# Optimization experiments

Measured on AMD Instinct MI355X. Metric: run time of the kernel, lower is better.

Reference implementation:

```python
import jax, jax.numpy as jnp
import numpy as np
import math

NUM_POSE_FEAT = 64  # -> pos emb dim 128
N_NBR = 16
TEMP = 10000.0


def pos2posemb2d(pos, num_pos_feats=NUM_POSE_FEAT):
    # PETR-style 2D sine embedding; pos: (..., 2) in [0,1)
    scale = 2.0 * math.pi
    pos = pos * scale
    dim_t = jnp.arange(num_pos_feats, dtype=pos.dtype)
    dim_t = TEMP ** (2.0 * jnp.floor(dim_t / 2.0) / num_pos_feats)
    pos_x = pos[..., 0:1] / dim_t  # (..., P)
    pos_y = pos[..., 1:2] / dim_t

    def interleave(p):
        return jnp.stack([jnp.sin(p[..., 0::2]), jnp.cos(p[..., 1::2])], axis=-1).reshape(p.shape[:-1] + (-1,))

    return jnp.concatenate([interleave(pos_y), interleave(pos_x)], axis=-1)  # (..., 2P)


def mlp(x, W1, b1, W2, b2):
    return jax.nn.relu(x @ W1 + b1) @ W2 + b2


def setup_inputs() -> dict:
    key = jax.random.key(0)
    ks = jax.random.split(key, 12)
    B, S, L, D, P2 = 4, 4096, 8192, 256, 2 * NUM_POSE_FEAT
    s1 = 1.0 / np.sqrt(P2)
    s2 = 1.0 / np.sqrt(D)
    return {
        "memory": jax.random.normal(ks[0], (B, L, D), jnp.float32),
        "mem_coor": jax.random.uniform(ks[1], (B, L, 2), dtype=jnp.float32),
        "q_coor": jax.random.uniform(ks[2], (B, S, 2), dtype=jnp.float32),
        "Wq1": jax.random.normal(ks[3], (P2, D), jnp.float32) * s1,
        "bq1": jnp.zeros((D,), jnp.float32),
        "Wq2": jax.random.normal(ks[4], (D, D), jnp.float32) * s2,
        "bq2": jnp.zeros((D,), jnp.float32),
        "Wk1": jax.random.normal(ks[5], (P2, D), jnp.float32) * s1,
        "bk1": jnp.zeros((D,), jnp.float32),
        "Wk2": jax.random.normal(ks[6], (D, D), jnp.float32) * s2,
        "bk2": jnp.zeros((D,), jnp.float32),
        "B": 4,
    }


def reference(memory, mem_coor, q_coor, Wq1, bq1, Wq2, bq2, Wk1, bk1, Wk2, bk2, B):
    # memory: (B, L, D); mem_coor: (B, L, 2); q_coor: (B, S, 2)
    Bn, L, D = memory.shape
    query = mlp(pos2posemb2d(q_coor), Wq1, bq1, Wq2, bq2)      # (B, S, D) query = query_pos
    mem_pos = mlp(pos2posemb2d(mem_coor), Wk1, bk1, Wk2, bk2)  # (B, L, D)
    kv_pe = mem_pos + memory                                   # (B, L, D)

    # squared pairwise distances via matmul expansion (monotonic in true distance,
    # only the top-k ORDER is consumed downstream)
    q2 = jnp.sum(q_coor * q_coor, axis=-1)                     # (B, S)
    m2 = jnp.sum(mem_coor * mem_coor, axis=-1)                 # (B, L)
    d2 = q2[:, :, None] + m2[:, None, :] - 2.0 * jnp.einsum("bsc,blc->bsl", q_coor, mem_coor)
    _, idx = jax.lax.top_k(-d2, N_NBR)                         # (B, S, k) nearest-neighbor indices

    bidx = jnp.arange(Bn)[:, None, None]
    kv_m = kv_pe[bidx, idx]                                    # (B, S, k, D) gathered pos-embedded memory
    prod = query[:, :, None, :] * kv_m / jnp.sqrt(jnp.asarray(D, query.dtype))
    attn = jax.nn.softmax(prod, axis=-1)                       # softmax over feature dim D
    out = attn * memory[bidx, idx]                             # (B, S, k, D)
    return out
```

## Files before the change

kernel.cpp:

```cpp
#include <hip/hip_runtime.h>
#include <math.h>

#define NB 4
#define NS 4096
#define NL 8192
#define ND 256
#define NP2 128
#define NK 16

#define GCELLS 32
#define GH 0.03125f
#define CAP 256
#define EPSM 2e-5f

__device__ __forceinline__ float sum_sq_np(float x, float y) {
#pragma clang fp contract(off)
  return x * x + y * y;
}

__device__ __forceinline__ float dist2_fast(float q2, float m2, float qx, float qy,
                                            float mx, float my) {
#pragma clang fp contract(off)
  float dot = __builtin_fmaf(qy, my, qx * mx);
  float s = q2 + m2;
  return __builtin_fmaf(-2.0f, dot, s);
}

__device__ __forceinline__ unsigned f32ord(float f) {
  unsigned u = __float_as_uint(f);
  return u ^ ((unsigned)((int)u >> 31) | 0x80000000u);
}

template <int NR>
__device__ __forceinline__ unsigned extract16(const unsigned long long* candrow,
                                              int cnt, int lane,
                                              int* __restrict__ outp) {
  unsigned long long myc[NR];
#pragma unroll
  for (int j = 0; j < NR; ++j) {
    int p = lane + j * 64;
    myc[j] = (p < cnt) ? candrow[p] : ~0ull;
  }
  unsigned tau_ord = 0xffffffffu;
#pragma unroll 1
  for (int r = 0; r < NK; ++r) {
    unsigned long long m = myc[0];
#pragma unroll
    for (int j = 1; j < NR; ++j) m = myc[j] < m ? myc[j] : m;
#pragma unroll
    for (int o = 1; o < 64; o <<= 1) {
      unsigned long long other = __shfl_xor(m, o, 64);
      if (other < m) m = other;
    }
    if (lane == 0) outp[r] = (int)(unsigned)(m & 0xffffffffull);
    if (r == NK - 1) tau_ord = (unsigned)(m >> 32);
#pragma unroll
    for (int j = 0; j < NR; ++j)
      if (myc[j] == m) myc[j] = ~0ull;
  }
  return tau_ord;
}

#define RPAD 20
#define NSBLK (NB * NS / 16)

struct __align__(16) MlpSmem {
  float pe[NP2][RPAD];
  float h[ND][RPAD];
};

__device__ __forceinline__ void fma16(float* acc, float wt, const float4& p0,
                                      const float4& p1, const float4& p2,
                                      const float4& p3) {
  acc[0] = fmaf(p0.x, wt, acc[0]);   acc[1] = fmaf(p0.y, wt, acc[1]);
  acc[2] = fmaf(p0.z, wt, acc[2]);   acc[3] = fmaf(p0.w, wt, acc[3]);
  acc[4] = fmaf(p1.x, wt, acc[4]);   acc[5] = fmaf(p1.y, wt, acc[5]);
  acc[6] = fmaf(p1.z, wt, acc[6]);   acc[7] = fmaf(p1.w, wt, acc[7]);
  acc[8] = fmaf(p2.x, wt, acc[8]);   acc[9] = fmaf(p2.y, wt, acc[9]);
  acc[10] = fmaf(p2.z, wt, acc[10]); acc[11] = fmaf(p2.w, wt, acc[11]);
  acc[12] = fmaf(p3.x, wt, acc[12]); acc[13] = fmaf(p3.y, wt, acc[13]);
  acc[14] = fmaf(p3.z, wt, acc[14]); acc[15] = fmaf(p3.w, wt, acc[15]);
}

__device__ __forceinline__ void loadW8(const float* __restrict__ W, int k0,
                                       int tid, float* w0, float* w1) {
#pragma unroll
  for (int u = 0; u < 8; ++u) {
    w0[u] = W[(size_t)(k0 + u) * ND + tid];
    w1[u] = W[(size_t)(k0 + u) * ND + 128 + tid];
  }
}

__device__ __forceinline__ void consume8(const float (*L)[RPAD], int k0,
                                         const float* w0, const float* w1,
                                         float* acc0, float* acc1) {
#pragma unroll
  for (int u = 0; u < 8; ++u) {
    int k = k0 + u;
    float4 p0 = *(const float4*)&L[k][0];
    float4 p1 = *(const float4*)&L[k][4];
    float4 p2 = *(const float4*)&L[k][8];
    float4 p3 = *(const float4*)&L[k][12];
    fma16(acc0, w0[u], p0, p1, p2, p3);
    fma16(acc1, w1[u], p0, p1, p2, p3);
  }
}

__global__ __launch_bounds__(128) void mlp_fused_kernel(
    const float* __restrict__ q_coor, const float* __restrict__ mem_coor,
    const float* __restrict__ memory,
    const float* __restrict__ Wq1, const float* __restrict__ bq1,
    const float* __restrict__ Wq2, const float* __restrict__ bq2,
    const float* __restrict__ Wk1, const float* __restrict__ bk1,
    const float* __restrict__ Wk2, const float* __restrict__ bk2,
    float* __restrict__ query, float* __restrict__ kv_pe) {
  __shared__ MlpSmem sm;
  const int tid = threadIdx.x;
  const int bid = blockIdx.x;
  const bool isS = bid < NSBLK;
  const float* coor = isS ? q_coor : mem_coor;
  const float* W1 = isS ? Wq1 : Wk1;
  const float* b1 = isS ? bq1 : bk1;
  const float* W2 = isS ? Wq2 : Wk2;
  const float* b2 = isS ? bq2 : bk2;
  const float* addmem = isS ? (const float*)nullptr : memory;
  float* out = isS ? query : kv_pe;
  const int row0 = (isS ? bid : bid - NSBLK) * 16;

#pragma unroll
  for (int it = 0; it < 8; ++it) {
    int e = tid + it * 128;
    int r = e >> 6;
    int rem = e & 63;
    int part = rem >> 5;
    int j = rem & 31;
    float c = coor[(size_t)(row0 + r) * 2 + (part ^ 1)];
    float inv_t = exp2f((float)j * -0.4152410118609718f);
    float arg = c * 6.2831853071795864f * inv_t;
    float sv, cv;
    sincosf(arg, &sv, &cv);
    int k0 = part * 64 + 2 * j;
    sm.pe[k0][r] = sv;
    sm.pe[k0 + 1][r] = cv;
  }
  __syncthreads();

  float acc0[16], acc1[16];
  float wA0[8], wA1[8], wB0[8], wB1[8];
  {
    float bb0 = b1[tid], bb1 = b1[tid + 128];
#pragma unroll
    for (int r = 0; r < 16; ++r) { acc0[r] = bb0; acc1[r] = bb1; }
  }
  loadW8(W1, 0, tid, wA0, wA1);
#pragma unroll 1
  for (int k0 = 0; k0 < NP2; k0 += 16) {
    loadW8(W1, k0 + 8, tid, wB0, wB1);
    consume8(sm.pe, k0, wA0, wA1, acc0, acc1);
    if (k0 + 16 < NP2) loadW8(W1, k0 + 16, tid, wA0, wA1);
    consume8(sm.pe, k0 + 8, wB0, wB1, acc0, acc1);
  }
#pragma unroll
  for (int r = 0; r < 16; ++r) {
    sm.h[tid][r] = fmaxf(acc0[r], 0.0f);
    sm.h[tid + 128][r] = fmaxf(acc1[r], 0.0f);
  }
  __syncthreads();

  {
    float bb0 = b2[tid], bb1 = b2[tid + 128];
#pragma unroll
    for (int r = 0; r < 16; ++r) { acc0[r] = bb0; acc1[r] = bb1; }
  }
  loadW8(W2, 0, tid, wA0, wA1);
#pragma unroll 1
  for (int k0 = 0; k0 < ND; k0 += 16) {
    loadW8(W2, k0 + 8, tid, wB0, wB1);
    consume8(sm.h, k0, wA0, wA1, acc0, acc1);
    if (k0 + 16 < ND) loadW8(W2, k0 + 16, tid, wA0, wA1);
    consume8(sm.h, k0 + 8, wB0, wB1, acc0, acc1);
  }
#pragma unroll
  for (int r = 0; r < 16; ++r) {
    size_t g = (size_t)(row0 + r);
    float v0 = acc0[r], v1 = acc1[r];
    if (addmem) {
      v0 += addmem[g * ND + tid];
      v1 += addmem[g * ND + 128 + tid];
    }
    out[g * ND + tid] = v0;
    out[g * ND + 128 + tid] = v1;
  }
}

__global__ __launch_bounds__(1024) void grid_build_kernel(
    const float* __restrict__ mem_coor, float4* __restrict__ sorted,
    int* __restrict__ starts) {
  __shared__ int hist[GCELLS * GCELLS];
  __shared__ int cur[GCELLS * GCELLS];
  const int b = blockIdx.x;
  const int tid = threadIdx.x;
  const float2* mc = (const float2*)mem_coor + (size_t)b * NL;

  hist[tid] = 0;
  __syncthreads();
#pragma unroll
  for (int it = 0; it < NL / 1024; ++it) {
    float2 c = mc[it * 1024 + tid];
    int cx = (int)(c.x * 32.0f); cx = cx > 31 ? 31 : cx;
    int cy = (int)(c.y * 32.0f); cy = cy > 31 ? 31 : cy;
    atomicAdd(&hist[cy * GCELLS + cx], 1);
  }
  __syncthreads();
  const int own = hist[tid];
  for (int o = 1; o < 1024; o <<= 1) {
    int v = (tid >= o) ? hist[tid - o] : 0;
    __syncthreads();
    hist[tid] += v;
    __syncthreads();
  }
  const int excl = hist[tid] - own;
  starts[b * (GCELLS * GCELLS + 1) + tid] = excl;
  if (tid == 0) starts[b * (GCELLS * GCELLS + 1) + GCELLS * GCELLS] = NL;
  cur[tid] = excl;
  __syncthreads();
#pragma unroll
  for (int it = 0; it < NL / 1024; ++it) {
    int i = it * 1024 + tid;
    float2 c = mc[i];
    int cx = (int)(c.x * 32.0f); cx = cx > 31 ? 31 : cx;
    int cy = (int)(c.y * 32.0f); cy = cy > 31 ? 31 : cy;
    int pos = atomicAdd(&cur[cy * GCELLS + cx], 1);
    sorted[(size_t)b * NL + pos] =
        make_float4(c.x, c.y, sum_sq_np(c.x, c.y), __int_as_float(i));
  }
}

__global__ __launch_bounds__(256) void topk_kernel(
    const float* __restrict__ q_coor, const float4* __restrict__ sorted,
    const int* __restrict__ starts, int* __restrict__ idx_out) {
  __shared__ unsigned long long cand[4][CAP];
  __shared__ int fcnt[4];

  const int tid = threadIdx.x;
  const int wv = tid >> 6;
  const int lane = tid & 63;
  const int qi = blockIdx.x * 4 + wv;
  const int b = qi >> 12;

  const float qx = q_coor[(size_t)qi * 2 + 0];
  const float qy = q_coor[(size_t)qi * 2 + 1];
  const float q2 = sum_sq_np(qx, qy);
  const float4* sp = sorted + (size_t)b * NL;
  const int* st = starts + b * (GCELLS * GCELLS + 1);
  int* outp = idx_out + (size_t)qi * NK;

  int ci = (int)(qx * 32.0f); ci = ci > 31 ? 31 : ci;
  int cj = (int)(qy * 32.0f); cj = cj > 31 ? 31 : cj;

  int x0 = ci - 1 < 0 ? 0 : ci - 1, x1 = ci + 1 > 31 ? 31 : ci + 1;
  int y0 = cj - 1 < 0 ? 0 : cj - 1, y1 = cj + 1 > 31 ? 31 : cj + 1;
  int cnt = 0;
  bool ovf = false;

  auto span = [&](int y, int xa, int xb) {
    int s0 = st[y * GCELLS + xa];
    int e0 = st[y * GCELLS + xb + 1];
    int len = e0 - s0;
    if (cnt + len > CAP) { ovf = true; return; }
    for (int i = lane; i < len; i += 64) {
      float4 rx = sp[s0 + i];
      float d2 = dist2_fast(q2, rx.z, qx, qy, rx.x, rx.y);
      cand[wv][cnt + i] = ((unsigned long long)f32ord(d2) << 32) |
                          (unsigned)__float_as_int(rx.w);
    }
    cnt += len;
  };

  for (int y = y0; y <= y1 && !ovf; ++y) span(y, x0, x1);

  int R = 1;
  while (!ovf) {
    unsigned tau_ord;
    if (cnt <= 128) tau_ord = extract16<2>(cand[wv], cnt, lane, outp);
    else            tau_ord = extract16<4>(cand[wv], cnt, lane, outp);
    float dxl = x0 > 0  ? qx - (float)x0 * GH        : 1e30f;
    float dxr = x1 < 31 ? (float)(x1 + 1) * GH - qx  : 1e30f;
    float dyl = y0 > 0  ? qy - (float)y0 * GH        : 1e30f;
    float dyr = y1 < 31 ? (float)(y1 + 1) * GH - qy  : 1e30f;
    float dmin = fminf(fminf(dxl, dxr), fminf(dyl, dyr));
    float bound = dmin * dmin - EPSM;
    if (cnt >= NK && tau_ord < f32ord(bound)) return;
    if (x0 == 0 && x1 == 31 && y0 == 0 && y1 == 31) return;
    ++R;
    int nx0 = ci - R < 0 ? 0 : ci - R, nx1 = ci + R > 31 ? 31 : ci + R;
    int ny0 = cj - R < 0 ? 0 : cj - R, ny1 = cj + R > 31 ? 31 : cj + R;
    if (ny0 < y0) span(ny0, nx0, nx1);
    if (ny1 > y1 && !ovf) span(ny1, nx0, nx1);
    for (int y = y0; y <= y1 && !ovf; ++y) {
      if (nx0 < x0) span(y, nx0, x0 - 1);
      if (nx1 > x1 && !ovf) span(y, x1 + 1, nx1);
    }
    x0 = nx0; x1 = nx1; y0 = ny0; y1 = ny1;
  }

  float lmin = __builtin_inff();
#pragma unroll 8
  for (int it = 0; it < NL / 64; ++it) {
    float4 rx = sp[it * 64 + lane];
    float d2 = dist2_fast(q2, rx.z, qx, qy, rx.x, rx.y);
    lmin = fminf(lmin, d2);
  }
  float tau;
  {
    float curm = lmin;
    for (int r = 0; r < NK; ++r) {
      float m = curm;
#pragma unroll
      for (int o = 1; o < 64; o <<= 1) m = fminf(m, __shfl_xor(m, o, 64));
      tau = m;
      if (curm == m) curm = __builtin_inff();
    }
  }
  if (lane == 0) fcnt[wv] = 0;
#pragma unroll 4
  for (int it = 0; it < NL / 64; ++it) {
    float4 rx = sp[it * 64 + lane];
    float d2 = dist2_fast(q2, rx.z, qx, qy, rx.x, rx.y);
    bool hit = (d2 <= tau);
    unsigned long long mask = __ballot(hit);
    if (mask) {
      int base = fcnt[wv];
      if (hit) {
        int pos = base + (int)__popcll(mask & ((1ull << lane) - 1ull));
        if (pos < CAP) {
          cand[wv][pos] = ((unsigned long long)f32ord(d2) << 32) |
                          (unsigned)__float_as_int(rx.w);
        }
      }
      if (lane == 0) fcnt[wv] = base + (int)__popcll(mask);
    }
  }
  int N = fcnt[wv];
  if (N > CAP) N = CAP;
  extract16<4>(cand[wv], N, lane, outp);
}

__global__ __launch_bounds__(256) void attn_kernel(
    const float* __restrict__ query, const float* __restrict__ kv_pe,
    const float* __restrict__ memory, const int* __restrict__ idx,
    float* __restrict__ out) {
  const int tid = threadIdx.x;
  const int wv = tid >> 6;
  const int lane = tid & 63;
  const int qi = blockIdx.x * 4 + wv;
  const int b = qi >> 12;

  float4 q4 = *(const float4*)(query + (size_t)qi * ND + lane * 4);
  int lv = 0;
  if (lane < NK) lv = idx[(size_t)qi * NK + lane];

#pragma unroll 4
  for (int k = 0; k < NK; ++k) {
    int l = __shfl(lv, k, 64);
    size_t base = ((size_t)b * NL + l) * ND + (size_t)lane * 4;
    float4 kv = *(const float4*)(kv_pe + base);
    float4 mm = *(const float4*)(memory + base);
    float p0 = q4.x * kv.x * 0.0625f;
    float p1 = q4.y * kv.y * 0.0625f;
    float p2 = q4.z * kv.z * 0.0625f;
    float p3 = q4.w * kv.w * 0.0625f;
    float mx = fmaxf(fmaxf(p0, p1), fmaxf(p2, p3));
#pragma unroll
    for (int o = 1; o < 64; o <<= 1) mx = fmaxf(mx, __shfl_xor(mx, o, 64));
    float e0 = expf(p0 - mx);
    float e1 = expf(p1 - mx);
    float e2 = expf(p2 - mx);
    float e3 = expf(p3 - mx);
    float s = (e0 + e1) + (e2 + e3);
#pragma unroll
    for (int o = 1; o < 64; o <<= 1) s += __shfl_xor(s, o, 64);
    float inv = 1.0f / s;
    float4 o4;
    o4.x = e0 * inv * mm.x;
    o4.y = e1 * inv * mm.y;
    o4.z = e2 * inv * mm.z;
    o4.w = e3 * inv * mm.w;
    *(float4*)(out + ((size_t)qi * NK + k) * ND + (size_t)lane * 4) = o4;
  }
}

extern "C" void kernel_launch(void* const* d_in, const int* in_sizes, int n_in,
                              void* d_out, int out_size, void* d_ws, size_t ws_size,
                              hipStream_t stream) {
  (void)in_sizes; (void)n_in; (void)out_size; (void)ws_size;
  const float* memory   = (const float*)d_in[0];
  const float* mem_coor = (const float*)d_in[1];
  const float* q_coor   = (const float*)d_in[2];
  const float* Wq1 = (const float*)d_in[3];
  const float* bq1 = (const float*)d_in[4];
  const float* Wq2 = (const float*)d_in[5];
  const float* bq2 = (const float*)d_in[6];
  const float* Wk1 = (const float*)d_in[7];
  const float* bk1 = (const float*)d_in[8];
  const float* Wk2 = (const float*)d_in[9];
  const float* bk2 = (const float*)d_in[10];

  float* query = (float*)d_ws;
  float* kv_pe = query + (size_t)NB * NS * ND;
  int*   nidx  = (int*)(kv_pe + (size_t)NB * NL * ND);
  float* outp  = (float*)d_out;

  float4* sorted  = (float4*)d_out;
  int*    gstarts = (int*)((char*)d_out + (size_t)NB * NL * 16);

  hipLaunchKernelGGL(grid_build_kernel, dim3(NB), dim3(1024), 0, stream,
                     mem_coor, sorted, gstarts);
  hipLaunchKernelGGL(mlp_fused_kernel, dim3(NSBLK + NB * NL / 16), dim3(128),
                     0, stream, q_coor, mem_coor, memory,
                     Wq1, bq1, Wq2, bq2, Wk1, bk1, Wk2, bk2, query, kv_pe);
  hipLaunchKernelGGL(topk_kernel, dim3(NB * NS / 4), dim3(256), 0, stream,
                     q_coor, sorted, gstarts, nidx);
  hipLaunchKernelGGL(attn_kernel, dim3(NB * NS / 4), dim3(256), 0, stream,
                     query, kv_pe, memory, nidx, outp);
}
```

Baseline: 576.9 us.

## Process attention queries in spatial grid order and shrink MLP shared memory

```diff
diff --git a/kernel.cpp b/kernel.cpp
--- a/kernel.cpp
+++ b/kernel.cpp
@@ -65,8 +65,10 @@
 #define NSBLK (NB * NS / 16)
 
 struct __align__(16) MlpSmem {
-  float pe[NP2][RPAD];
-  float h[ND][RPAD];
+  union {
+    float pe[NP2][RPAD];
+    float h[ND][RPAD];
+  };
 };
 
 __device__ __forceinline__ void fma16(float* acc, float wt, const float4& p0,
@@ -106,7 +108,7 @@
   }
 }
 
-__global__ __launch_bounds__(128) void mlp_fused_kernel(
+__global__ __launch_bounds__(128, 4) void mlp_fused_kernel(
     const float* __restrict__ q_coor, const float* __restrict__ mem_coor,
     const float* __restrict__ memory,
     const float* __restrict__ Wq1, const float* __restrict__ bq1,
@@ -160,6 +162,7 @@
     if (k0 + 16 < NP2) loadW8(W1, k0 + 16, tid, wA0, wA1);
     consume8(sm.pe, k0 + 8, wB0, wB1, acc0, acc1);
   }
+  __syncthreads();
 #pragma unroll
   for (int r = 0; r < 16; ++r) {
     sm.h[tid][r] = fmaxf(acc0[r], 0.0f);
@@ -193,20 +196,23 @@
   }
 }
 
-__global__ __launch_bounds__(1024) void grid_build_kernel(
-    const float* __restrict__ mem_coor, float4* __restrict__ sorted,
-    int* __restrict__ starts) {
+__global__ __launch_bounds__(1024) void build_kernel(
+    const float* __restrict__ mem_coor, const float* __restrict__ q_coor,
+    float4* __restrict__ sorted, int* __restrict__ starts,
+    int* __restrict__ qord) {
   __shared__ int hist[GCELLS * GCELLS];
   __shared__ int cur[GCELLS * GCELLS];
-  const int b = blockIdx.x;
+  const int bid = blockIdx.x;
+  const bool isMem = bid < NB;
+  const int b = isMem ? bid : bid - NB;
+  const int n = isMem ? NL : NS;
+  const float2* cc = (const float2*)(isMem ? mem_coor : q_coor) + (size_t)b * n;
   const int tid = threadIdx.x;
-  const float2* mc = (const float2*)mem_coor + (size_t)b * NL;
 
   hist[tid] = 0;
   __syncthreads();
-#pragma unroll
-  for (int it = 0; it < NL / 1024; ++it) {
-    float2 c = mc[it * 1024 + tid];
+  for (int it = 0; it < n / 1024; ++it) {
+    float2 c = cc[it * 1024 + tid];
     int cx = (int)(c.x * 32.0f); cx = cx > 31 ? 31 : cx;
     int cy = (int)(c.y * 32.0f); cy = cy > 31 ? 31 : cy;
     atomicAdd(&hist[cy * GCELLS + cx], 1);
@@ -220,19 +226,24 @@
     __syncthreads();
   }
   const int excl = hist[tid] - own;
-  starts[b * (GCELLS * GCELLS + 1) + tid] = excl;
-  if (tid == 0) starts[b * (GCELLS * GCELLS + 1) + GCELLS * GCELLS] = NL;
+  if (isMem) {
+    starts[b * (GCELLS * GCELLS + 1) + tid] = excl;
+    if (tid == 0) starts[b * (GCELLS * GCELLS + 1) + GCELLS * GCELLS] = NL;
+  }
   cur[tid] = excl;
   __syncthreads();
-#pragma unroll
-  for (int it = 0; it < NL / 1024; ++it) {
+  for (int it = 0; it < n / 1024; ++it) {
     int i = it * 1024 + tid;
-    float2 c = mc[i];
+    float2 c = cc[i];
     int cx = (int)(c.x * 32.0f); cx = cx > 31 ? 31 : cx;
     int cy = (int)(c.y * 32.0f); cy = cy > 31 ? 31 : cy;
     int pos = atomicAdd(&cur[cy * GCELLS + cx], 1);
-    sorted[(size_t)b * NL + pos] =
-        make_float4(c.x, c.y, sum_sq_np(c.x, c.y), __int_as_float(i));
+    if (isMem) {
+      sorted[(size_t)b * NL + pos] =
+          make_float4(c.x, c.y, sum_sq_np(c.x, c.y), __int_as_float(i));
+    } else {
+      qord[b * NS + pos] = i;
+    }
   }
 }
 
@@ -349,12 +360,14 @@
 __global__ __launch_bounds__(256) void attn_kernel(
     const float* __restrict__ query, const float* __restrict__ kv_pe,
     const float* __restrict__ memory, const int* __restrict__ idx,
-    float* __restrict__ out) {
+    const int* __restrict__ qord, float* __restrict__ out) {
   const int tid = threadIdx.x;
   const int wv = tid >> 6;
   const int lane = tid & 63;
-  const int qi = blockIdx.x * 4 + wv;
-  const int b = qi >> 12;
+  const int bid = ((blockIdx.x & 7) * (NB * NS / 4 / 8)) + (blockIdx.x >> 3);
+  const int qpos = bid * 4 + wv;
+  const int b = qpos >> 12;
+  const int qi = b * NS + qord[qpos];
 
   float4 q4 = *(const float4*)(query + (size_t)qi * ND + lane * 4);
   int lv = 0;
@@ -409,18 +422,19 @@
   float* query = (float*)d_ws;
   float* kv_pe = query + (size_t)NB * NS * ND;
   int*   nidx  = (int*)(kv_pe + (size_t)NB * NL * ND);
+  int*   qord  = nidx + (size_t)NB * NS * NK;
   float* outp  = (float*)d_out;
 
   float4* sorted  = (float4*)d_out;
   int*    gstarts = (int*)((char*)d_out + (size_t)NB * NL * 16);
 
-  hipLaunchKernelGGL(grid_build_kernel, dim3(NB), dim3(1024), 0, stream,
-                     mem_coor, sorted, gstarts);
+  hipLaunchKernelGGL(build_kernel, dim3(2 * NB), dim3(1024), 0, stream,
+                     mem_coor, q_coor, sorted, gstarts, qord);
   hipLaunchKernelGGL(mlp_fused_kernel, dim3(NSBLK + NB * NL / 16), dim3(128),
                      0, stream, q_coor, mem_coor, memory,
                      Wq1, bq1, Wq2, bq2, Wk1, bk1, Wk2, bk2, query, kv_pe);
   hipLaunchKernelGGL(topk_kernel, dim3(NB * NS / 4), dim3(256), 0, stream,
                      q_coor, sorted, gstarts, nidx);
   hipLaunchKernelGGL(attn_kernel, dim3(NB * NS / 4), dim3(256), 0, stream,
-                     query, kv_pe, memory, nidx, outp);
-}
+                     query, kv_pe, memory, nidx, qord, outp);
+}
```

Result: slower. 1.588 ms (+175.3%).
